# Kernel tuning notes

Hardware: AMD Instinct MI355X
Metric: run time of the kernel (lower is better)

Reference implementation:

```python
import jax, jax.numpy as jnp
import numpy as np

B, L, C = 8, 2048, 512
CI = C // 2  # internal_units


def setup_inputs() -> dict:
    key = jax.random.key(0)
    ks = jax.random.split(key, 4)
    inputs = jax.random.normal(ks[0], (B, L, C), dtype=jnp.float32)
    # Conv1D kernel_size=1 == per-position linear; kernel_initializer='random_normal' (stddev 0.05)
    Wx = 0.05 * jax.random.normal(ks[1], (C, CI), dtype=jnp.float32)
    Wy = 0.05 * jax.random.normal(ks[2], (C, CI), dtype=jnp.float32)
    Wo = 0.05 * jax.random.normal(ks[3], (C, C), dtype=jnp.float32)
    bx = jnp.zeros((CI,), dtype=jnp.float32)
    by = jnp.zeros((CI,), dtype=jnp.float32)
    bo = jnp.zeros((C,), dtype=jnp.float32)
    return {"inputs": inputs, "Wx": Wx, "bx": bx, "Wy": Wy, "by": by, "Wo": Wo, "bo": bo}


def reference(inputs, Wx, bx, Wy, by, Wo, bo):
    # 1x1 conv projections (per-position linear layers with bias)
    x_proj = jnp.einsum('blc,ci->bli', inputs, Wx) + bx   # [B, L, Ci]
    y_proj = jnp.einsum('blc,ci->bli', inputs, Wy) + by   # [B, L, Ci]
    o_proj = jnp.einsum('blc,cd->bld', inputs, Wo) + bo   # [B, L, C]
    # scores: batched matmul x @ y^T -> [B, L, L]
    scores = jnp.einsum('bli,bmi->blm', x_proj, y_proj)
    # NOTE: softmax over axis=0 (the BATCH axis), as in the original module
    attn = jax.nn.softmax(scores, axis=0)
    s_dot = jnp.einsum('blm,bmc->blc', attn, o_proj)       # [B, L, C]
    return inputs + s_dot
```

## Files before the change

### kernel.cpp

```cpp
#include <hip/hip_runtime.h>


#define NB 8
#define NL 2048
#define NC 512
#define NCI 256

using f16x8 = __attribute__((ext_vector_type(8))) _Float16;
using f32x4 = __attribute__((ext_vector_type(4))) float;
typedef unsigned short u16;

__device__ __forceinline__ u16 f16b(float x) {
    _Float16 h = (_Float16)x;
    return __builtin_bit_cast(u16, h);
}
__device__ __forceinline__ void gload16(const void* g, void* l) {
    __builtin_amdgcn_global_load_lds((__attribute__((address_space(1))) void*)g,
                                     (__attribute__((address_space(3))) void*)l,
                                     16, 0, 0);
}

__global__ __launch_bounds__(256) void cvt_x_kernel(const float* __restrict__ X,
                                                    u16* __restrict__ Xf)
{
    size_t i = (size_t)blockIdx.x * 256 + threadIdx.x;
    const float4* X4 = (const float4*)X;
    float4 a = X4[2 * i], b = X4[2 * i + 1];
    u16 o[8] = {f16b(a.x), f16b(a.y), f16b(a.z), f16b(a.w),
                f16b(b.x), f16b(b.y), f16b(b.z), f16b(b.w)};
    ((uint4*)Xf)[i] = *(const uint4*)o;
}

__global__ __launch_bounds__(256) void cvt_w_kernel(
    const float* __restrict__ Wx, const float* __restrict__ Wy, const float* __restrict__ Wo,
    u16* __restrict__ WxT, u16* __restrict__ WyT, u16* __restrict__ WoT)
{
    const int bid = blockIdx.x, t = threadIdx.x;
#pragma unroll
    for (int kk = 0; kk < 2; ++kk) {
        const int k = t + kk * 256;
        if (bid < 256)      WxT[(size_t)bid * NC + k] = f16b(Wx[(size_t)k * NCI + bid]);
        else if (bid < 512) WyT[(size_t)(bid - 256) * NC + k] = f16b(Wy[(size_t)k * NCI + (bid - 256)]);
        else                WoT[(size_t)(bid - 512) * NC + k] = f16b(Wo[(size_t)k * NC + (bid - 512)]);
    }
}

__global__ __launch_bounds__(256) void proj_kernel(
    const u16* __restrict__ Xf,
    const u16* __restrict__ WxT, const u16* __restrict__ WyT, const u16* __restrict__ WoT,
    const float* __restrict__ bx, const float* __restrict__ by, const float* __restrict__ bo,
    u16* __restrict__ xp, u16* __restrict__ yp, u16* __restrict__ opT)
{
    __shared__ __align__(16) u16 SM[17408];
    u16* As = SM;
    u16* Bs = SM + 8192;

    const int tid = threadIdx.x;
    const int w = tid >> 6, lane = tid & 63;
    const int row0 = blockIdx.x * 128;
    const int cb = blockIdx.y;

    const u16* W; const float* bias; int n0, path;
    if (cb < 2)      { path = 0; n0 = cb * 128;       W = WxT; bias = bx; }
    else if (cb < 4) { path = 1; n0 = (cb - 2) * 128; W = WyT; bias = by; }
    else             { path = 2; n0 = (cb - 4) * 128; W = WoT; bias = bo; }

    f32x4 acc[4][4] = {};
    const int wm = (w & 1) * 64, wn = (w >> 1) * 64;
    const int fr = lane & 15, fq = lane >> 4;

    for (int k0 = 0; k0 < NC; k0 += 64) {
#pragma unroll
        for (int pass = 0; pass < 4; ++pass) {
            const int cbase = pass * 256 + w * 64;
            const int chunk = cbase + lane;
            const int r = chunk >> 3;
            const int kc = (chunk & 7) ^ (r & 7);
            gload16(Xf + (size_t)(row0 + r) * NC + k0 + kc * 8, (char*)As + cbase * 16);
            gload16(W  + (size_t)(n0  + r) * NC + k0 + kc * 8, (char*)Bs + cbase * 16);
        }
        __syncthreads();
        f16x8 a[4][2], b[4][2];
#pragma unroll
        for (int mi = 0; mi < 4; ++mi)
#pragma unroll
            for (int kt = 0; kt < 2; ++kt)
                a[mi][kt] = *(const f16x8*)&As[(wm + mi * 16 + fr) * 64 + ((kt * 4 + fq) ^ (fr & 7)) * 8];
#pragma unroll
        for (int ni = 0; ni < 4; ++ni)
#pragma unroll
            for (int kt = 0; kt < 2; ++kt)
                b[ni][kt] = *(const f16x8*)&Bs[(wn + ni * 16 + fr) * 64 + ((kt * 4 + fq) ^ (fr & 7)) * 8];
#pragma unroll
        for (int kt = 0; kt < 2; ++kt)
#pragma unroll
            for (int mi = 0; mi < 4; ++mi)
#pragma unroll
                for (int ni = 0; ni < 4; ++ni)
                    acc[mi][ni] = __builtin_amdgcn_mfma_f32_16x16x32_f16(a[mi][kt], b[ni][kt], acc[mi][ni], 0, 0, 0);
        __syncthreads();
    }

    if (path != 2) {
        u16* O = (path == 0) ? xp : yp;
#pragma unroll
        for (int mi = 0; mi < 4; ++mi) {
            const int grow = row0 + wm + mi * 16 + fq * 4;
#pragma unroll
            for (int ni = 0; ni < 4; ++ni) {
                const int gcol = n0 + wn + ni * 16 + fr;
                const float bv = bias[gcol];
#pragma unroll
                for (int r = 0; r < 4; ++r)
                    O[(size_t)(grow + r) * NCI + gcol] = f16b(acc[mi][ni][r] + bv);
            }
        }
    } else {
        u16* Ts = SM;
#pragma unroll
        for (int mi = 0; mi < 4; ++mi) {
            const int mb = wm + mi * 16 + fq * 4;
#pragma unroll
            for (int ni = 0; ni < 4; ++ni) {
                const int nl_ = wn + ni * 16 + fr;
                const float bv = bias[n0 + nl_];
#pragma unroll
                for (int r = 0; r < 4; ++r)
                    Ts[nl_ * 136 + mb + r] = f16b(acc[mi][ni][r] + bv);
            }
        }
        __syncthreads();
        const int b = row0 >> 11, m0 = row0 & 2047;
        u16* dst = opT + (size_t)b * NC * NL + (size_t)n0 * NL + m0;
        for (int i = tid; i < 128 * 16; i += 256) {
            const int c = i >> 4, ch = i & 15;
            uint4 v = *(const uint4*)&Ts[c * 136 + ch * 8];
            *(uint4*)&dst[(size_t)c * NL + ch * 8] = v;
        }
    }
}

__global__ __launch_bounds__(256) void score_kernel(
    const u16* __restrict__ xp, const u16* __restrict__ yp, u16* __restrict__ S16)
{
    __shared__ __align__(16) u16 As[8192], Bs[8192];
    const int tid = threadIdx.x;
    const int w = tid >> 6, lane = tid & 63;
    const int b = blockIdx.z;
    const int row0 = blockIdx.x * 128, col0 = blockIdx.y * 128;
    const size_t ab = (size_t)b * NL * NCI;
    const u16* A = xp + ab;
    const u16* B = yp + ab;

    f32x4 acc[4][4] = {};
    const int wm = (w & 1) * 64, wn = (w >> 1) * 64;
    const int fr = lane & 15, fq = lane >> 4;

    for (int k0 = 0; k0 < NCI; k0 += 64) {
#pragma unroll
        for (int pass = 0; pass < 4; ++pass) {
            const int cbase = pass * 256 + w * 64;
            const int chunk = cbase + lane;
            const int r = chunk >> 3;
            const int kc = (chunk & 7) ^ (r & 7);
            gload16(A + (size_t)(row0 + r) * NCI + k0 + kc * 8, (char*)As + cbase * 16);
            gload16(B + (size_t)(col0 + r) * NCI + k0 + kc * 8, (char*)Bs + cbase * 16);
        }
        __syncthreads();
        f16x8 a[4][2], bfr[4][2];
#pragma unroll
        for (int mi = 0; mi < 4; ++mi)
#pragma unroll
            for (int kt = 0; kt < 2; ++kt)
                a[mi][kt] = *(const f16x8*)&As[(wm + mi * 16 + fr) * 64 + ((kt * 4 + fq) ^ (fr & 7)) * 8];
#pragma unroll
        for (int ni = 0; ni < 4; ++ni)
#pragma unroll
            for (int kt = 0; kt < 2; ++kt)
                bfr[ni][kt] = *(const f16x8*)&Bs[(wn + ni * 16 + fr) * 64 + ((kt * 4 + fq) ^ (fr & 7)) * 8];
#pragma unroll
        for (int kt = 0; kt < 2; ++kt)
#pragma unroll
            for (int mi = 0; mi < 4; ++mi)
#pragma unroll
                for (int ni = 0; ni < 4; ++ni)
                    acc[mi][ni] = __builtin_amdgcn_mfma_f32_16x16x32_f16(a[mi][kt], bfr[ni][kt], acc[mi][ni], 0, 0, 0);
        __syncthreads();
    }
    u16* Sb = S16 + (size_t)b * NL * NL;
#pragma unroll
    for (int mi = 0; mi < 4; ++mi) {
        const int gr = row0 + wm + mi * 16 + fq * 4;
#pragma unroll
        for (int ni = 0; ni < 4; ++ni) {
            const int gc = col0 + wn + ni * 16 + fr;
#pragma unroll
            for (int r = 0; r < 4; ++r)
                Sb[(size_t)(gr + r) * NL + gc] = f16b(acc[mi][ni][r]);
        }
    }
}

__global__ __launch_bounds__(256) void softmax_kernel(u16* __restrict__ S16)
{
    const size_t g = (size_t)blockIdx.x * 256 + threadIdx.x;
    const size_t st = (size_t)NL * NL / 8;
    uint4* P = (uint4*)S16;
    uint4 raw[NB];
#pragma unroll
    for (int b = 0; b < NB; ++b) raw[b] = P[b * st + g];
    float f[NB][8];
#pragma unroll
    for (int b = 0; b < NB; ++b) {
        f16x8 h = __builtin_bit_cast(f16x8, raw[b]);
#pragma unroll
        for (int j = 0; j < 8; ++j) f[b][j] = (float)h[j];
    }
#pragma unroll
    for (int j = 0; j < 8; ++j) {
        float mx = f[0][j];
#pragma unroll
        for (int b = 1; b < NB; ++b) mx = fmaxf(mx, f[b][j]);
        float s = 0.f;
#pragma unroll
        for (int b = 0; b < NB; ++b) { f[b][j] = __expf(f[b][j] - mx); s += f[b][j]; }
        const float inv = 1.f / s;
#pragma unroll
        for (int b = 0; b < NB; ++b) f[b][j] *= inv;
    }
#pragma unroll
    for (int b = 0; b < NB; ++b) {
        u16 o[8];
#pragma unroll
        for (int j = 0; j < 8; ++j) o[j] = f16b(f[b][j]);
        P[b * st + g] = *(const uint4*)o;
    }
}

__global__ __launch_bounds__(512) void out_kernel(
    const u16* __restrict__ S16, const u16* __restrict__ opT,
    const float* __restrict__ X, float* __restrict__ Out)
{
    __shared__ __align__(16) u16 As[8192], Bs[8192];
    const int tid = threadIdx.x;
    const int w = tid >> 6, lane = tid & 63;
    const int b = blockIdx.z;
    const int row0 = blockIdx.x * 128, col0 = blockIdx.y * 128;
    const u16* Aatt = S16 + (size_t)b * NL * NL;
    const u16* Bsrc = opT + (size_t)b * NC * NL;

    f32x4 acc[4][2] = {};
    const int wm = (w & 1) * 64, wn = (w >> 1) * 32;
    const int fr = lane & 15, fq = lane >> 4;

    for (int k0 = 0; k0 < NL; k0 += 64) {
#pragma unroll
        for (int pass = 0; pass < 2; ++pass) {
            const int cbase = pass * 512 + w * 64;
            const int chunk = cbase + lane;
            const int r = chunk >> 3;
            const int kc = (chunk & 7) ^ (r & 7);
            gload16(Aatt + (size_t)(row0 + r) * NL + k0 + kc * 8, (char*)As + cbase * 16);
            gload16(Bsrc + (size_t)(col0 + r) * NL + k0 + kc * 8, (char*)Bs + cbase * 16);
        }
        __syncthreads();
        f16x8 af[4][2], bf[2][2];
#pragma unroll
        for (int mi = 0; mi < 4; ++mi)
#pragma unroll
            for (int kt = 0; kt < 2; ++kt)
                af[mi][kt] = *(const f16x8*)&As[(wm + mi * 16 + fr) * 64 + ((kt * 4 + fq) ^ (fr & 7)) * 8];
#pragma unroll
        for (int ni = 0; ni < 2; ++ni)
#pragma unroll
            for (int kt = 0; kt < 2; ++kt)
                bf[ni][kt] = *(const f16x8*)&Bs[(wn + ni * 16 + fr) * 64 + ((kt * 4 + fq) ^ (fr & 7)) * 8];
#pragma unroll
        for (int kt = 0; kt < 2; ++kt)
#pragma unroll
            for (int mi = 0; mi < 4; ++mi)
#pragma unroll
                for (int ni = 0; ni < 2; ++ni)
                    acc[mi][ni] = __builtin_amdgcn_mfma_f32_16x16x32_f16(af[mi][kt], bf[ni][kt], acc[mi][ni], 0, 0, 0);
        __syncthreads();
    }
    const size_t ob = (size_t)b * NL * NC;
#pragma unroll
    for (int mi = 0; mi < 4; ++mi) {
        const int gr = row0 + wm + mi * 16 + fq * 4;
#pragma unroll
        for (int ni = 0; ni < 2; ++ni) {
            const int gc = col0 + wn + ni * 16 + fr;
#pragma unroll
            for (int r = 0; r < 4; ++r) {
                const size_t o = ob + (size_t)(gr + r) * NC + gc;
                Out[o] = X[o] + acc[mi][ni][r];
            }
        }
    }
}

extern "C" void kernel_launch(void* const* d_in, const int* in_sizes, int n_in,
                              void* d_out, int out_size, void* d_ws, size_t ws_size,
                              hipStream_t stream)
{
    const float* X  = (const float*)d_in[0];
    const float* Wx = (const float*)d_in[1];
    const float* bx = (const float*)d_in[2];
    const float* Wy = (const float*)d_in[3];
    const float* by = (const float*)d_in[4];
    const float* Wo = (const float*)d_in[5];
    const float* bo = (const float*)d_in[6];
    float* out = (float*)d_out;

    char* ws = (char*)d_ws;
    u16* S16 = (u16*)ws;
    u16* Xf  = (u16*)ws;
    char* p = ws + 67108864;
    u16* xp  = (u16*)p; p += 8388608;
    u16* yp  = (u16*)p; p += 8388608;
    u16* opT = (u16*)p; p += 16777216;
    u16* WxT = (u16*)p; p += 262144;
    u16* WyT = (u16*)p; p += 262144;
    u16* WoT = (u16*)p; p += 524288;

    cvt_x_kernel<<<4096, 256, 0, stream>>>(X, Xf);
    cvt_w_kernel<<<1024, 256, 0, stream>>>(Wx, Wy, Wo, WxT, WyT, WoT);
    proj_kernel<<<dim3(128, 8), 256, 0, stream>>>(Xf, WxT, WyT, WoT, bx, by, bo, xp, yp, opT);
    score_kernel<<<dim3(16, 16, NB), 256, 0, stream>>>(xp, yp, S16);
    softmax_kernel<<<2048, 256, 0, stream>>>(S16);
    out_kernel<<<dim3(16, 4, NB), 512, 0, stream>>>(S16, opT, X, out);
}
```

Measured before the change: 219.8 us.

## Fuse score GEMM with batch-axis softmax and double-buffer out GEMM loads

Score computation and the batch-axis softmax are merged into one kernel. Each block computes a 64x64 score tile for all 8 batches, keeps the values in registers, and normalizes across batches before writing attention once. This removes the write and re-read of the full score tensor plus a kernel launch. The price is smaller tiles, less operand reuse, a serial loop over batches, and scattered 2-byte stores. The output GEMM also gains LDS double buffering, so the next tile's global-to-LDS load overlaps the current MFMAs and one barrier per iteration goes away.

```diff
diff --git a/kernel.cpp b/kernel.cpp
--- a/kernel.cpp
+++ b/kernel.cpp
@@ -13,6 +13,9 @@
 __device__ __forceinline__ u16 f16b(float x) {
     _Float16 h = (_Float16)x;
     return __builtin_bit_cast(u16, h);
+}
+__device__ __forceinline__ float f16tof(u16 u) {
+    return (float)__builtin_bit_cast(_Float16, u);
 }
 __device__ __forceinline__ void gload16(const void* g, void* l) {
     __builtin_amdgcn_global_load_lds((__attribute__((address_space(1))) void*)g,
@@ -140,141 +143,134 @@
     }
 }
 
-__global__ __launch_bounds__(256) void score_kernel(
-    const u16* __restrict__ xp, const u16* __restrict__ yp, u16* __restrict__ S16)
-{
-    __shared__ __align__(16) u16 As[8192], Bs[8192];
+__global__ __launch_bounds__(256) void score_softmax_kernel(
+    const u16* __restrict__ xp, const u16* __restrict__ yp, u16* __restrict__ ATT)
+{
+    __shared__ __align__(16) u16 As[4096], Bs[4096];
+    const int tid = threadIdx.x;
+    const int w = tid >> 6, lane = tid & 63;
+    const int row0 = blockIdx.x * 64, col0 = blockIdx.y * 64;
+    const int wn = w * 16;
+    const int fr = lane & 15, fq = lane >> 4;
+
+    unsigned sv[NB][8];
+
+#pragma unroll
+    for (int b = 0; b < NB; ++b) {
+        const u16* A = xp + (size_t)b * NL * NCI;
+        const u16* B = yp + (size_t)b * NL * NCI;
+        f32x4 acc[4] = {};
+        for (int k0 = 0; k0 < NCI; k0 += 64) {
+#pragma unroll
+            for (int pass = 0; pass < 2; ++pass) {
+                const int cbase = pass * 256 + w * 64;
+                const int chunk = cbase + lane;
+                const int r = chunk >> 3;
+                const int kc = (chunk & 7) ^ (r & 7);
+                gload16(A + (size_t)(row0 + r) * NCI + k0 + kc * 8, (char*)As + cbase * 16);
+                gload16(B + (size_t)(col0 + r) * NCI + k0 + kc * 8, (char*)Bs + cbase * 16);
+            }
+            __syncthreads();
+            f16x8 af[4][2], bf[2];
+#pragma unroll
+            for (int mi = 0; mi < 4; ++mi)
+#pragma unroll
+                for (int kt = 0; kt < 2; ++kt)
+                    af[mi][kt] = *(const f16x8*)&As[(mi * 16 + fr) * 64 + ((kt * 4 + fq) ^ (fr & 7)) * 8];
+#pragma unroll
+            for (int kt = 0; kt < 2; ++kt)
+                bf[kt] = *(const f16x8*)&Bs[(wn + fr) * 64 + ((kt * 4 + fq) ^ (fr & 7)) * 8];
+#pragma unroll
+            for (int kt = 0; kt < 2; ++kt)
+#pragma unroll
+                for (int mi = 0; mi < 4; ++mi)
+                    acc[mi] = __builtin_amdgcn_mfma_f32_16x16x32_f16(af[mi][kt], bf[kt], acc[mi], 0, 0, 0);
+            __syncthreads();
+        }
+#pragma unroll
+        for (int mi = 0; mi < 4; ++mi) {
+            sv[b][mi * 2 + 0] = (unsigned)f16b(acc[mi][0]) | ((unsigned)f16b(acc[mi][1]) << 16);
+            sv[b][mi * 2 + 1] = (unsigned)f16b(acc[mi][2]) | ((unsigned)f16b(acc[mi][3]) << 16);
+        }
+    }
+
+    const int gc = col0 + wn + fr;
+#pragma unroll
+    for (int mi = 0; mi < 4; ++mi) {
+#pragma unroll
+        for (int rp = 0; rp < 2; ++rp) {
+            float v0[NB], v1[NB];
+#pragma unroll
+            for (int b = 0; b < NB; ++b) {
+                unsigned u = sv[b][mi * 2 + rp];
+                v0[b] = f16tof((u16)(u & 0xFFFF));
+                v1[b] = f16tof((u16)(u >> 16));
+            }
+            float m0 = v0[0], m1 = v1[0];
+#pragma unroll
+            for (int b = 1; b < NB; ++b) { m0 = fmaxf(m0, v0[b]); m1 = fmaxf(m1, v1[b]); }
+            float s0 = 0.f, s1 = 0.f;
+#pragma unroll
+            for (int b = 0; b < NB; ++b) {
+                v0[b] = __expf(v0[b] - m0); s0 += v0[b];
+                v1[b] = __expf(v1[b] - m1); s1 += v1[b];
+            }
+            const float i0 = 1.f / s0, i1 = 1.f / s1;
+            const int gr0 = row0 + mi * 16 + fq * 4 + rp * 2;
+#pragma unroll
+            for (int b = 0; b < NB; ++b) {
+                u16* dst = ATT + (size_t)b * NL * NL;
+                dst[(size_t)gr0 * NL + gc]       = f16b(v0[b] * i0);
+                dst[(size_t)(gr0 + 1) * NL + gc] = f16b(v1[b] * i1);
+            }
+        }
+    }
+}
+
+__global__ __launch_bounds__(512) void out_kernel(
+    const u16* __restrict__ ATT, const u16* __restrict__ opT,
+    const float* __restrict__ X, float* __restrict__ Out)
+{
+    __shared__ __align__(16) u16 As[2][8192], Bs[2][8192];
     const int tid = threadIdx.x;
     const int w = tid >> 6, lane = tid & 63;
     const int b = blockIdx.z;
     const int row0 = blockIdx.x * 128, col0 = blockIdx.y * 128;
-    const size_t ab = (size_t)b * NL * NCI;
-    const u16* A = xp + ab;
-    const u16* B = yp + ab;
-
-    f32x4 acc[4][4] = {};
-    const int wm = (w & 1) * 64, wn = (w >> 1) * 64;
-    const int fr = lane & 15, fq = lane >> 4;
-
-    for (int k0 = 0; k0 < NCI; k0 += 64) {
-#pragma unroll
-        for (int pass = 0; pass < 4; ++pass) {
-            const int cbase = pass * 256 + w * 64;
-            const int chunk = cbase + lane;
-            const int r = chunk >> 3;
-            const int kc = (chunk & 7) ^ (r & 7);
-            gload16(A + (size_t)(row0 + r) * NCI + k0 + kc * 8, (char*)As + cbase * 16);
-            gload16(B + (size_t)(col0 + r) * NCI + k0 + kc * 8, (char*)Bs + cbase * 16);
-        }
-        __syncthreads();
-        f16x8 a[4][2], bfr[4][2];
-#pragma unroll
-        for (int mi = 0; mi < 4; ++mi)
-#pragma unroll
-            for (int kt = 0; kt < 2; ++kt)
-                a[mi][kt] = *(const f16x8*)&As[(wm + mi * 16 + fr) * 64 + ((kt * 4 + fq) ^ (fr & 7)) * 8];
-#pragma unroll
-        for (int ni = 0; ni < 4; ++ni)
-#pragma unroll
-            for (int kt = 0; kt < 2; ++kt)
-                bfr[ni][kt] = *(const f16x8*)&Bs[(wn + ni * 16 + fr) * 64 + ((kt * 4 + fq) ^ (fr & 7)) * 8];
-#pragma unroll
-        for (int kt = 0; kt < 2; ++kt)
-#pragma unroll
-            for (int mi = 0; mi < 4; ++mi)
-#pragma unroll
-                for (int ni = 0; ni < 4; ++ni)
-                    acc[mi][ni] = __builtin_amdgcn_mfma_f32_16x16x32_f16(a[mi][kt], bfr[ni][kt], acc[mi][ni], 0, 0, 0);
-        __syncthreads();
-    }
-    u16* Sb = S16 + (size_t)b * NL * NL;
-#pragma unroll
-    for (int mi = 0; mi < 4; ++mi) {
-        const int gr = row0 + wm + mi * 16 + fq * 4;
-#pragma unroll
-        for (int ni = 0; ni < 4; ++ni) {
-            const int gc = col0 + wn + ni * 16 + fr;
-#pragma unroll
-            for (int r = 0; r < 4; ++r)
-                Sb[(size_t)(gr + r) * NL + gc] = f16b(acc[mi][ni][r]);
-        }
-    }
-}
-
-__global__ __launch_bounds__(256) void softmax_kernel(u16* __restrict__ S16)
-{
-    const size_t g = (size_t)blockIdx.x * 256 + threadIdx.x;
-    const size_t st = (size_t)NL * NL / 8;
-    uint4* P = (uint4*)S16;
-    uint4 raw[NB];
-#pragma unroll
-    for (int b = 0; b < NB; ++b) raw[b] = P[b * st + g];
-    float f[NB][8];
-#pragma unroll
-    for (int b = 0; b < NB; ++b) {
-        f16x8 h = __builtin_bit_cast(f16x8, raw[b]);
-#pragma unroll
-        for (int j = 0; j < 8; ++j) f[b][j] = (float)h[j];
-    }
-#pragma unroll
-    for (int j = 0; j < 8; ++j) {
-        float mx = f[0][j];
-#pragma unroll
-        for (int b = 1; b < NB; ++b) mx = fmaxf(mx, f[b][j]);
-        float s = 0.f;
-#pragma unroll
-        for (int b = 0; b < NB; ++b) { f[b][j] = __expf(f[b][j] - mx); s += f[b][j]; }
-        const float inv = 1.f / s;
-#pragma unroll
-        for (int b = 0; b < NB; ++b) f[b][j] *= inv;
-    }
-#pragma unroll
-    for (int b = 0; b < NB; ++b) {
-        u16 o[8];
-#pragma unroll
-        for (int j = 0; j < 8; ++j) o[j] = f16b(f[b][j]);
-        P[b * st + g] = *(const uint4*)o;
-    }
-}
-
-__global__ __launch_bounds__(512) void out_kernel(
-    const u16* __restrict__ S16, const u16* __restrict__ opT,
-    const float* __restrict__ X, float* __restrict__ Out)
-{
-    __shared__ __align__(16) u16 As[8192], Bs[8192];
-    const int tid = threadIdx.x;
-    const int w = tid >> 6, lane = tid & 63;
-    const int b = blockIdx.z;
-    const int row0 = blockIdx.x * 128, col0 = blockIdx.y * 128;
-    const u16* Aatt = S16 + (size_t)b * NL * NL;
+    const u16* Aatt = ATT + (size_t)b * NL * NL;
     const u16* Bsrc = opT + (size_t)b * NC * NL;
 
     f32x4 acc[4][2] = {};
     const int wm = (w & 1) * 64, wn = (w >> 1) * 32;
     const int fr = lane & 15, fq = lane >> 4;
 
-    for (int k0 = 0; k0 < NL; k0 += 64) {
+    auto stage = [&](int k0, int bu) {
 #pragma unroll
         for (int pass = 0; pass < 2; ++pass) {
             const int cbase = pass * 512 + w * 64;
             const int chunk = cbase + lane;
             const int r = chunk >> 3;
             const int kc = (chunk & 7) ^ (r & 7);
-            gload16(Aatt + (size_t)(row0 + r) * NL + k0 + kc * 8, (char*)As + cbase * 16);
-            gload16(Bsrc + (size_t)(col0 + r) * NL + k0 + kc * 8, (char*)Bs + cbase * 16);
-        }
+            gload16(Aatt + (size_t)(row0 + r) * NL + k0 + kc * 8, (char*)&As[bu][0] + cbase * 16);
+            gload16(Bsrc + (size_t)(col0 + r) * NL + k0 + kc * 8, (char*)&Bs[bu][0] + cbase * 16);
+        }
+    };
+
+    stage(0, 0);
+    int bu = 0;
+    for (int it = 0; it < NL / 64; ++it) {
         __syncthreads();
+        if (it + 1 < NL / 64) stage((it + 1) * 64, bu ^ 1);
         f16x8 af[4][2], bf[2][2];
 #pragma unroll
         for (int mi = 0; mi < 4; ++mi)
 #pragma unroll
             for (int kt = 0; kt < 2; ++kt)
-                af[mi][kt] = *(const f16x8*)&As[(wm + mi * 16 + fr) * 64 + ((kt * 4 + fq) ^ (fr & 7)) * 8];
+                af[mi][kt] = *(const f16x8*)&As[bu][(wm + mi * 16 + fr) * 64 + ((kt * 4 + fq) ^ (fr & 7)) * 8];
 #pragma unroll
         for (int ni = 0; ni < 2; ++ni)
 #pragma unroll
             for (int kt = 0; kt < 2; ++kt)
-                bf[ni][kt] = *(const f16x8*)&Bs[(wn + ni * 16 + fr) * 64 + ((kt * 4 + fq) ^ (fr & 7)) * 8];
+                bf[ni][kt] = *(const f16x8*)&Bs[bu][(wn + ni * 16 + fr) * 64 + ((kt * 4 + fq) ^ (fr & 7)) * 8];
 #pragma unroll
         for (int kt = 0; kt < 2; ++kt)
 #pragma unroll
@@ -282,7 +278,7 @@
 #pragma unroll
                 for (int ni = 0; ni < 2; ++ni)
                     acc[mi][ni] = __builtin_amdgcn_mfma_f32_16x16x32_f16(af[mi][kt], bf[ni][kt], acc[mi][ni], 0, 0, 0);
-        __syncthreads();
+        bu ^= 1;
     }
     const size_t ob = (size_t)b * NL * NC;
 #pragma unroll
@@ -314,7 +310,7 @@
     float* out = (float*)d_out;
 
     char* ws = (char*)d_ws;
-    u16* S16 = (u16*)ws;
+    u16* ATT = (u16*)ws;
     u16* Xf  = (u16*)ws;
     char* p = ws + 67108864;
     u16* xp  = (u16*)p; p += 8388608;
@@ -327,7 +323,6 @@
     cvt_x_kernel<<<4096, 256, 0, stream>>>(X, Xf);
     cvt_w_kernel<<<1024, 256, 0, stream>>>(Wx, Wy, Wo, WxT, WyT, WoT);
     proj_kernel<<<dim3(128, 8), 256, 0, stream>>>(Xf, WxT, WyT, WoT, bx, by, bo, xp, yp, opT);
-    score_kernel<<<dim3(16, 16, NB), 256, 0, stream>>>(xp, yp, S16);
-    softmax_kernel<<<2048, 256, 0, stream>>>(S16);
-    out_kernel<<<dim3(16, 4, NB), 512, 0, stream>>>(S16, opT, X, out);
-}
+    score_softmax_kernel<<<dim3(32, 32), 256, 0, stream>>>(xp, yp, ATT);
+    out_kernel<<<dim3(16, 4, NB), 512, 0, stream>>>(ATT, opT, X, out);
+}
```

Result: no change. 216.8 us (-1.4%).

## Double-buffer LDS tiles in GEMM kernels, merge convert kernels, stage score stores

Applied to the files above, without the earlier changes.

The three GEMM kernels (proj, score, out) now use double-buffered LDS tiles with K=32 steps. Each iteration issues the next tile's global-to-LDS loads before computing on the current one, which cuts one barrier per iteration and overlaps memory with MFMA work. The score kernel moves to 512 threads and writes its tile through LDS so global stores are coalesced 16-byte writes. The two conversion kernels become a single launch. Halving the K step doubles the number of loop iterations and barriers, and the new swizzle pattern could change LDS bank conflicts.

```diff
diff --git a/kernel.cpp b/kernel.cpp
--- a/kernel.cpp
+++ b/kernel.cpp
@@ -20,28 +20,28 @@
                                      16, 0, 0);
 }
 
-__global__ __launch_bounds__(256) void cvt_x_kernel(const float* __restrict__ X,
-                                                    u16* __restrict__ Xf)
-{
-    size_t i = (size_t)blockIdx.x * 256 + threadIdx.x;
-    const float4* X4 = (const float4*)X;
-    float4 a = X4[2 * i], b = X4[2 * i + 1];
-    u16 o[8] = {f16b(a.x), f16b(a.y), f16b(a.z), f16b(a.w),
-                f16b(b.x), f16b(b.y), f16b(b.z), f16b(b.w)};
-    ((uint4*)Xf)[i] = *(const uint4*)o;
-}
-
-__global__ __launch_bounds__(256) void cvt_w_kernel(
+__global__ __launch_bounds__(256) void cvt_kernel(
+    const float* __restrict__ X, u16* __restrict__ Xf,
     const float* __restrict__ Wx, const float* __restrict__ Wy, const float* __restrict__ Wo,
     u16* __restrict__ WxT, u16* __restrict__ WyT, u16* __restrict__ WoT)
 {
-    const int bid = blockIdx.x, t = threadIdx.x;
-#pragma unroll
-    for (int kk = 0; kk < 2; ++kk) {
-        const int k = t + kk * 256;
-        if (bid < 256)      WxT[(size_t)bid * NC + k] = f16b(Wx[(size_t)k * NCI + bid]);
-        else if (bid < 512) WyT[(size_t)(bid - 256) * NC + k] = f16b(Wy[(size_t)k * NCI + (bid - 256)]);
-        else                WoT[(size_t)(bid - 512) * NC + k] = f16b(Wo[(size_t)k * NC + (bid - 512)]);
+    const int bid = blockIdx.x;
+    if (bid < 4096) {
+        size_t i = (size_t)bid * 256 + threadIdx.x;
+        const float4* X4 = (const float4*)X;
+        float4 a = X4[2 * i], b = X4[2 * i + 1];
+        u16 o[8] = {f16b(a.x), f16b(a.y), f16b(a.z), f16b(a.w),
+                    f16b(b.x), f16b(b.y), f16b(b.z), f16b(b.w)};
+        ((uint4*)Xf)[i] = *(const uint4*)o;
+    } else {
+        const int wb = bid - 4096, t = threadIdx.x;
+#pragma unroll
+        for (int kk = 0; kk < 2; ++kk) {
+            const int k = t + kk * 256;
+            if (wb < 256)      WxT[(size_t)wb * NC + k] = f16b(Wx[(size_t)k * NCI + wb]);
+            else if (wb < 512) WyT[(size_t)(wb - 256) * NC + k] = f16b(Wy[(size_t)k * NCI + (wb - 256)]);
+            else               WoT[(size_t)(wb - 512) * NC + k] = f16b(Wo[(size_t)k * NC + (wb - 512)]);
+        }
     }
 }
 
@@ -52,9 +52,6 @@
     u16* __restrict__ xp, u16* __restrict__ yp, u16* __restrict__ opT)
 {
     __shared__ __align__(16) u16 SM[17408];
-    u16* As = SM;
-    u16* Bs = SM + 8192;
-
     const int tid = threadIdx.x;
     const int w = tid >> 6, lane = tid & 63;
     const int row0 = blockIdx.x * 128;
@@ -69,36 +66,44 @@
     const int wm = (w & 1) * 64, wn = (w >> 1) * 64;
     const int fr = lane & 15, fq = lane >> 4;
 
-    for (int k0 = 0; k0 < NC; k0 += 64) {
-#pragma unroll
-        for (int pass = 0; pass < 4; ++pass) {
+    auto stage = [&](int k0, int bu) {
+#pragma unroll
+        for (int pass = 0; pass < 2; ++pass) {
             const int cbase = pass * 256 + w * 64;
             const int chunk = cbase + lane;
-            const int r = chunk >> 3;
-            const int kc = (chunk & 7) ^ (r & 7);
-            gload16(Xf + (size_t)(row0 + r) * NC + k0 + kc * 8, (char*)As + cbase * 16);
-            gload16(W  + (size_t)(n0  + r) * NC + k0 + kc * 8, (char*)Bs + cbase * 16);
-        }
-        __syncthreads();
-        f16x8 a[4][2], b[4][2];
+            const int r = chunk >> 2;
+            const int kc = (chunk & 3) ^ ((r >> 1) & 3);
+            gload16(Xf + (size_t)(row0 + r) * NC + k0 + kc * 8,
+                    (char*)(SM + bu * 4096) + cbase * 16);
+            gload16(W  + (size_t)(n0  + r) * NC + k0 + kc * 8,
+                    (char*)(SM + 8192 + bu * 4096) + cbase * 16);
+        }
+    };
+
+    stage(0, 0);
+    int bu = 0;
+    for (int it = 0; it < NC / 32; ++it) {
+        __syncthreads();
+        if (it + 1 < NC / 32) stage((it + 1) * 32, bu ^ 1);
+        const u16* As = SM + bu * 4096;
+        const u16* Bs = SM + 8192 + bu * 4096;
+        f16x8 a[4], b[4];
+#pragma unroll
+        for (int mi = 0; mi < 4; ++mi) {
+            const int row = wm + mi * 16 + fr;
+            a[mi] = *(const f16x8*)&As[row * 32 + (fq ^ ((row >> 1) & 3)) * 8];
+        }
+#pragma unroll
+        for (int ni = 0; ni < 4; ++ni) {
+            const int row = wn + ni * 16 + fr;
+            b[ni] = *(const f16x8*)&Bs[row * 32 + (fq ^ ((row >> 1) & 3)) * 8];
+        }
 #pragma unroll
         for (int mi = 0; mi < 4; ++mi)
 #pragma unroll
-            for (int kt = 0; kt < 2; ++kt)
-                a[mi][kt] = *(const f16x8*)&As[(wm + mi * 16 + fr) * 64 + ((kt * 4 + fq) ^ (fr & 7)) * 8];
-#pragma unroll
-        for (int ni = 0; ni < 4; ++ni)
-#pragma unroll
-            for (int kt = 0; kt < 2; ++kt)
-                b[ni][kt] = *(const f16x8*)&Bs[(wn + ni * 16 + fr) * 64 + ((kt * 4 + fq) ^ (fr & 7)) * 8];
-#pragma unroll
-        for (int kt = 0; kt < 2; ++kt)
-#pragma unroll
-            for (int mi = 0; mi < 4; ++mi)
-#pragma unroll
-                for (int ni = 0; ni < 4; ++ni)
-                    acc[mi][ni] = __builtin_amdgcn_mfma_f32_16x16x32_f16(a[mi][kt], b[ni][kt], acc[mi][ni], 0, 0, 0);
-        __syncthreads();
+            for (int ni = 0; ni < 4; ++ni)
+                acc[mi][ni] = __builtin_amdgcn_mfma_f32_16x16x32_f16(a[mi], b[ni], acc[mi][ni], 0, 0, 0);
+        bu ^= 1;
     }
 
     if (path != 2) {
@@ -116,6 +121,7 @@
             }
         }
     } else {
+        __syncthreads();
         u16* Ts = SM;
 #pragma unroll
         for (int mi = 0; mi < 4; ++mi) {
@@ -140,10 +146,10 @@
     }
 }
 
-__global__ __launch_bounds__(256) void score_kernel(
+__global__ __launch_bounds__(512) void score_kernel(
     const u16* __restrict__ xp, const u16* __restrict__ yp, u16* __restrict__ S16)
 {
-    __shared__ __align__(16) u16 As[8192], Bs[8192];
+    __shared__ __align__(16) u16 SM[17408];
     const int tid = threadIdx.x;
     const int w = tid >> 6, lane = tid & 63;
     const int b = blockIdx.z;
@@ -152,52 +158,65 @@
     const u16* A = xp + ab;
     const u16* B = yp + ab;
 
-    f32x4 acc[4][4] = {};
-    const int wm = (w & 1) * 64, wn = (w >> 1) * 64;
+    f32x4 acc[4][2] = {};
+    const int wm = (w & 1) * 64, wn = (w >> 1) * 32;
     const int fr = lane & 15, fq = lane >> 4;
 
-    for (int k0 = 0; k0 < NCI; k0 += 64) {
-#pragma unroll
-        for (int pass = 0; pass < 4; ++pass) {
-            const int cbase = pass * 256 + w * 64;
-            const int chunk = cbase + lane;
-            const int r = chunk >> 3;
-            const int kc = (chunk & 7) ^ (r & 7);
-            gload16(A + (size_t)(row0 + r) * NCI + k0 + kc * 8, (char*)As + cbase * 16);
-            gload16(B + (size_t)(col0 + r) * NCI + k0 + kc * 8, (char*)Bs + cbase * 16);
-        }
-        __syncthreads();
-        f16x8 a[4][2], bfr[4][2];
+    auto stage = [&](int k0, int bu) {
+        const int chunk = w * 64 + lane;
+        const int r = chunk >> 2;
+        const int kc = (chunk & 3) ^ ((r >> 1) & 3);
+        gload16(A + (size_t)(row0 + r) * NCI + k0 + kc * 8,
+                (char*)(SM + bu * 4096) + chunk * 16);
+        gload16(B + (size_t)(col0 + r) * NCI + k0 + kc * 8,
+                (char*)(SM + 8192 + bu * 4096) + chunk * 16);
+    };
+
+    stage(0, 0);
+    int bu = 0;
+    for (int it = 0; it < NCI / 32; ++it) {
+        __syncthreads();
+        if (it + 1 < NCI / 32) stage((it + 1) * 32, bu ^ 1);
+        const u16* As = SM + bu * 4096;
+        const u16* Bs = SM + 8192 + bu * 4096;
+        f16x8 af[4], bf[2];
+#pragma unroll
+        for (int mi = 0; mi < 4; ++mi) {
+            const int row = wm + mi * 16 + fr;
+            af[mi] = *(const f16x8*)&As[row * 32 + (fq ^ ((row >> 1) & 3)) * 8];
+        }
+#pragma unroll
+        for (int ni = 0; ni < 2; ++ni) {
+            const int row = wn + ni * 16 + fr;
+            bf[ni] = *(const f16x8*)&Bs[row * 32 + (fq ^ ((row >> 1) & 3)) * 8];
+        }
 #pragma unroll
         for (int mi = 0; mi < 4; ++mi)
 #pragma unroll
-            for (int kt = 0; kt < 2; ++kt)
-                a[mi][kt] = *(const f16x8*)&As[(wm + mi * 16 + fr) * 64 + ((kt * 4 + fq) ^ (fr & 7)) * 8];
-#pragma unroll
-        for (int ni = 0; ni < 4; ++ni)
-#pragma unroll
-            for (int kt = 0; kt < 2; ++kt)
-                bfr[ni][kt] = *(const f16x8*)&Bs[(wn + ni * 16 + fr) * 64 + ((kt * 4 + fq) ^ (fr & 7)) * 8];
-#pragma unroll
-        for (int kt = 0; kt < 2; ++kt)
-#pragma unroll
-            for (int mi = 0; mi < 4; ++mi)
-#pragma unroll
-                for (int ni = 0; ni < 4; ++ni)
-                    acc[mi][ni] = __builtin_amdgcn_mfma_f32_16x16x32_f16(a[mi][kt], bfr[ni][kt], acc[mi][ni], 0, 0, 0);
-        __syncthreads();
-    }
+            for (int ni = 0; ni < 2; ++ni)
+                acc[mi][ni] = __builtin_amdgcn_mfma_f32_16x16x32_f16(af[mi], bf[ni], acc[mi][ni], 0, 0, 0);
+        bu ^= 1;
+    }
+
+    __syncthreads();
+    u16* Ts = SM;
+#pragma unroll
+    for (int mi = 0; mi < 4; ++mi) {
+        const int lr = wm + mi * 16 + fq * 4;
+#pragma unroll
+        for (int ni = 0; ni < 2; ++ni) {
+            const int lc = wn + ni * 16 + fr;
+#pragma unroll
+            for (int r = 0; r < 4; ++r)
+                Ts[(lr + r) * 136 + lc] = f16b(acc[mi][ni][r]);
+        }
+    }
+    __syncthreads();
     u16* Sb = S16 + (size_t)b * NL * NL;
-#pragma unroll
-    for (int mi = 0; mi < 4; ++mi) {
-        const int gr = row0 + wm + mi * 16 + fq * 4;
-#pragma unroll
-        for (int ni = 0; ni < 4; ++ni) {
-            const int gc = col0 + wn + ni * 16 + fr;
-#pragma unroll
-            for (int r = 0; r < 4; ++r)
-                Sb[(size_t)(gr + r) * NL + gc] = f16b(acc[mi][ni][r]);
-        }
+    for (int i = tid; i < 128 * 16; i += 512) {
+        const int row = i >> 4, ch = i & 15;
+        uint4 v = *(const uint4*)&Ts[row * 136 + ch * 8];
+        *(uint4*)&Sb[(size_t)(row0 + row) * NL + col0 + ch * 8] = v;
     }
 }
 
@@ -238,51 +257,55 @@
 }
 
 __global__ __launch_bounds__(512) void out_kernel(
-    const u16* __restrict__ S16, const u16* __restrict__ opT,
+    const u16* __restrict__ ATT, const u16* __restrict__ opT,
     const float* __restrict__ X, float* __restrict__ Out)
 {
-    __shared__ __align__(16) u16 As[8192], Bs[8192];
+    __shared__ __align__(16) u16 SM[16384];
     const int tid = threadIdx.x;
     const int w = tid >> 6, lane = tid & 63;
     const int b = blockIdx.z;
     const int row0 = blockIdx.x * 128, col0 = blockIdx.y * 128;
-    const u16* Aatt = S16 + (size_t)b * NL * NL;
+    const u16* Aatt = ATT + (size_t)b * NL * NL;
     const u16* Bsrc = opT + (size_t)b * NC * NL;
 
     f32x4 acc[4][2] = {};
     const int wm = (w & 1) * 64, wn = (w >> 1) * 32;
     const int fr = lane & 15, fq = lane >> 4;
 
-    for (int k0 = 0; k0 < NL; k0 += 64) {
-#pragma unroll
-        for (int pass = 0; pass < 2; ++pass) {
-            const int cbase = pass * 512 + w * 64;
-            const int chunk = cbase + lane;
-            const int r = chunk >> 3;
-            const int kc = (chunk & 7) ^ (r & 7);
-            gload16(Aatt + (size_t)(row0 + r) * NL + k0 + kc * 8, (char*)As + cbase * 16);
-            gload16(Bsrc + (size_t)(col0 + r) * NL + k0 + kc * 8, (char*)Bs + cbase * 16);
-        }
-        __syncthreads();
-        f16x8 af[4][2], bf[2][2];
+    auto stage = [&](int k0, int bu) {
+        const int chunk = w * 64 + lane;
+        const int r = chunk >> 2;
+        const int kc = (chunk & 3) ^ ((r >> 1) & 3);
+        gload16(Aatt + (size_t)(row0 + r) * NL + k0 + kc * 8,
+                (char*)(SM + bu * 4096) + chunk * 16);
+        gload16(Bsrc + (size_t)(col0 + r) * NL + k0 + kc * 8,
+                (char*)(SM + 8192 + bu * 4096) + chunk * 16);
+    };
+
+    stage(0, 0);
+    int bu = 0;
+    for (int it = 0; it < NL / 32; ++it) {
+        __syncthreads();
+        if (it + 1 < NL / 32) stage((it + 1) * 32, bu ^ 1);
+        const u16* As = SM + bu * 4096;
+        const u16* Bs = SM + 8192 + bu * 4096;
+        f16x8 af[4], bf[2];
+#pragma unroll
+        for (int mi = 0; mi < 4; ++mi) {
+            const int row = wm + mi * 16 + fr;
+            af[mi] = *(const f16x8*)&As[row * 32 + (fq ^ ((row >> 1) & 3)) * 8];
+        }
+#pragma unroll
+        for (int ni = 0; ni < 2; ++ni) {
+            const int row = wn + ni * 16 + fr;
+            bf[ni] = *(const f16x8*)&Bs[row * 32 + (fq ^ ((row >> 1) & 3)) * 8];
+        }
 #pragma unroll
         for (int mi = 0; mi < 4; ++mi)
 #pragma unroll
-            for (int kt = 0; kt < 2; ++kt)
-                af[mi][kt] = *(const f16x8*)&As[(wm + mi * 16 + fr) * 64 + ((kt * 4 + fq) ^ (fr & 7)) * 8];
-#pragma unroll
-        for (int ni = 0; ni < 2; ++ni)
-#pragma unroll
-            for (int kt = 0; kt < 2; ++kt)
-                bf[ni][kt] = *(const f16x8*)&Bs[(wn + ni * 16 + fr) * 64 + ((kt * 4 + fq) ^ (fr & 7)) * 8];
-#pragma unroll
-        for (int kt = 0; kt < 2; ++kt)
-#pragma unroll
-            for (int mi = 0; mi < 4; ++mi)
-#pragma unroll
-                for (int ni = 0; ni < 2; ++ni)
-                    acc[mi][ni] = __builtin_amdgcn_mfma_f32_16x16x32_f16(af[mi][kt], bf[ni][kt], acc[mi][ni], 0, 0, 0);
-        __syncthreads();
+            for (int ni = 0; ni < 2; ++ni)
+                acc[mi][ni] = __builtin_amdgcn_mfma_f32_16x16x32_f16(af[mi], bf[ni], acc[mi][ni], 0, 0, 0);
+        bu ^= 1;
     }
     const size_t ob = (size_t)b * NL * NC;
 #pragma unroll
@@ -324,10 +347,9 @@
     u16* WyT = (u16*)p; p += 262144;
     u16* WoT = (u16*)p; p += 524288;
 
-    cvt_x_kernel<<<4096, 256, 0, stream>>>(X, Xf);
-    cvt_w_kernel<<<1024, 256, 0, stream>>>(Wx, Wy, Wo, WxT, WyT, WoT);
+    cvt_kernel<<<5120, 256, 0, stream>>>(X, Xf, Wx, Wy, Wo, WxT, WyT, WoT);
     proj_kernel<<<dim3(128, 8), 256, 0, stream>>>(Xf, WxT, WyT, WoT, bx, by, bo, xp, yp, opT);
-    score_kernel<<<dim3(16, 16, NB), 256, 0, stream>>>(xp, yp, S16);
+    score_kernel<<<dim3(16, 16, NB), 512, 0, stream>>>(xp, yp, S16);
     softmax_kernel<<<2048, 256, 0, stream>>>(S16);
     out_kernel<<<dim3(16, 4, NB), 512, 0, stream>>>(S16, opT, X, out);
 }
```

Result: no change. 219.1 us (-0.3%).
